# Kernel optimization log

Measured on AMD Instinct MI355X. Metric: run time of the kernel, lower is better.

## Reference

```python
import jax, jax.numpy as jnp
import numpy as np

B, S, E, H, L, OUT = 128, 256, 300, 512, 2, 2


def _lstm_dir(x, mask, w_ih, w_hh, b, h0, c0, reverse):
    """One direction of one LSTM layer with length masking (packed-seq semantics).
    x: [B,S,D], mask: [B,S] bool (t < length). Returns (outputs [B,S,H], final h [B,H]).
    For reverse=True, scan runs t=S-1..0; state only updates once t < length, which
    exactly reproduces pack_padded_sequence reverse-direction behavior.
    """
    def step(carry, inp):
        h, c = carry
        xt, mt = inp  # [B,D], [B]
        z = xt @ w_ih.T + h @ w_hh.T + b  # [B,4H], torch gate order i,f,g,o
        i, f, g, o = jnp.split(z, 4, axis=-1)
        c_new = jax.nn.sigmoid(f) * c + jax.nn.sigmoid(i) * jnp.tanh(g)
        h_new = jax.nn.sigmoid(o) * jnp.tanh(c_new)
        m = mt[:, None]
        h = jnp.where(m, h_new, h)
        c = jnp.where(m, c_new, c)
        return (h, c), h
    (hT, _), hs = jax.lax.scan(step, (h0, c0), (jnp.swapaxes(x, 0, 1), mask.T), reverse=reverse)
    return jnp.swapaxes(hs, 0, 1), hT


def setup_inputs():
    key = jax.random.key(0)
    ks = iter(jax.random.split(key, 32))
    lengths = jax.random.randint(next(ks), (B,), 1, S + 1)
    x = jax.random.normal(next(ks), (B, S, E), jnp.float32)
    # module encodes per-sample lengths in input[:, -1, 0]
    x = x.at[:, -1, 0].set(lengths.astype(jnp.float32))
    k = 1.0 / np.sqrt(H)
    def u(shape):
        return jax.random.uniform(next(ks), shape, jnp.float32, -k, k)
    d = {"x": x}
    for l in range(L):
        din = E if l == 0 else 2 * H
        for suf in ("f", "r"):
            d[f"w_ih_l{l}_{suf}"] = u((4 * H, din))
            d[f"w_hh_l{l}_{suf}"] = u((4 * H, H))
            d[f"b_ih_l{l}_{suf}"] = u((4 * H,))
            d[f"b_hh_l{l}_{suf}"] = u((4 * H,))
    d["fc1_w"] = u((H, H))
    d["fc1_b"] = u((H,))
    d["fc_w"] = u((OUT, H))
    d["fc_b"] = u((OUT,))
    return d


def _forward(x, params):
    Bx, Sx = x.shape[0], x.shape[1]
    lengths = jnp.minimum(x[:, -1, 0].astype(jnp.int32), Sx)  # clamp(max=seq_len)
    mask = jnp.arange(Sx)[None, :] < lengths[:, None]  # [B,S]
    h0 = jnp.ones((Bx, H), x.dtype)  # module uses ones, not zeros
    c0 = jnp.ones((Bx, H), x.dtype)
    inp = x
    hT_r = None
    for l in range(L):
        (wif, whf, bif, bhf), (wir, whr, bir, bhr) = params[l]
        out_f, _ = _lstm_dir(inp, mask, wif, whf, bif + bhf, h0, c0, False)
        out_r, hT_r = _lstm_dir(inp, mask, wir, whr, bir + bhr, h0, c0, True)
        inp = jnp.concatenate([out_f, out_r], axis=-1)  # [B,S,2H]
    # ht[-1] == final hidden of reverse direction of last layer
    return hT_r


def reference(x, w_ih_l0_f, w_hh_l0_f, b_ih_l0_f, b_hh_l0_f,
              w_ih_l0_r, w_hh_l0_r, b_ih_l0_r, b_hh_l0_r,
              w_ih_l1_f, w_hh_l1_f, b_ih_l1_f, b_hh_l1_f,
              w_ih_l1_r, w_hh_l1_r, b_ih_l1_r, b_hh_l1_r,
              fc1_w, fc1_b, fc_w, fc_b):
    params = [((w_ih_l0_f, w_hh_l0_f, b_ih_l0_f, b_hh_l0_f),
               (w_ih_l0_r, w_hh_l0_r, b_ih_l0_r, b_hh_l0_r)),
              ((w_ih_l1_f, w_hh_l1_f, b_ih_l1_f, b_hh_l1_f),
               (w_ih_l1_r, w_hh_l1_r, b_ih_l1_r, b_hh_l1_r))]
    ht = _forward(x, params)  # [B,H]
    out = ht @ fc1_w.T + fc1_b  # fc1 (no activation in original)
    return out @ fc_w.T + fc_b  # [B,OUT]
```

## Files before the change

kernel.cpp:

```cpp
#include <hip/hip_runtime.h>

#define B_  128
#define S_  256
#define E_  300
#define EP_ 320
#define H_  512
#define G_  2048
#define D1_ 1024
#define FSLOT_ 4
#define FA_WORDS_ (4*FSLOT_*4*32*32)
#define FC_WORDS_ (2*FSLOT_*4*32*32)

typedef _Float16 f16;
typedef __attribute__((ext_vector_type(8))) _Float16 f16x8;
typedef __attribute__((ext_vector_type(4))) float    f32x4;
typedef unsigned long long u64;
typedef unsigned int u32;

__device__ __forceinline__ float sigf(float x){ return 1.f/(1.f + __expf(-x)); }
__device__ __forceinline__ float tanhf_(float x){
  float e = __expf(-2.f*fabsf(x));
  float t = (1.f - e)/(1.f + e);
  return x < 0.f ? -t : t;
}

__device__ __forceinline__ u64 aload64(const u64* p){
  return __hip_atomic_load((u64*)p, __ATOMIC_RELAXED, __HIP_MEMORY_SCOPE_AGENT);
}
__device__ __forceinline__ u32 aload32(const u32* p){
  return __hip_atomic_load((u32*)p, __ATOMIC_RELAXED, __HIP_MEMORY_SCOPE_AGENT);
}
__device__ __forceinline__ void astore32(u32* p, u32 v){
  __hip_atomic_store(p, v, __ATOMIC_RELAXED, __HIP_MEMORY_SCOPE_AGENT);
}
union H8 { u64 q[2]; f16x8 v; };
union FU { f16 f; unsigned short s; };


__global__ void k_f32_to_f16(const float* __restrict__ s, f16* __restrict__ d, int n){
  int i = blockIdx.x*blockDim.x + threadIdx.x;
  if (i < n) d[i] = (f16)s[i];
}

__global__ void k_pad_w(const float* __restrict__ s, f16* __restrict__ d, int rows, int ks, int kd){
  int i = blockIdx.x*blockDim.x + threadIdx.x;
  if (i >= rows*kd) return;
  int r = i/kd, k = i - r*kd;
  d[i] = (k < ks) ? (f16)s[(size_t)r*ks + k] : (f16)0.f;
}

__global__ void k_bias(const float* __restrict__ a, const float* __restrict__ b,
                       float* __restrict__ d, int n){
  int i = blockIdx.x*blockDim.x + threadIdx.x;
  if (i < n) d[i] = a[i] + b[i];
}

__global__ void k_len(const float* __restrict__ x, int* __restrict__ len){
  int b = threadIdx.x;
  if (b < B_){
    int v = (int)x[((size_t)b*S_ + (S_-1))*E_];
    len[b] = v > S_ ? S_ : v;
  }
}

__global__ void k_zero(u32* __restrict__ p, int n){
  int i = blockIdx.x*blockDim.x + threadIdx.x;
  if (i < n) p[i] = 0u;
}

__global__ void k_init(f16* hxA, f16* hx1, float* cstate){
  int i = blockIdx.x*blockDim.x + threadIdx.x;
  if (i < B_*H_){
    hxA[i] = (f16)1.f;
    hxA[2*B_*H_ + i] = (f16)1.f;
    hx1[i] = (f16)1.f;
    cstate[i] = 1.f;
  }
}


__global__ __launch_bounds__(256) void k_gemm_bt(
    const f16* __restrict__ A, const f16* __restrict__ Bm,
    f16* __restrict__ C, const float* __restrict__ bias,
    int M, int N, int K)
{
  __shared__ f16 As[128*32];
  __shared__ f16 Bs[128*32];
  const int m0 = blockIdx.x*128, n0 = blockIdx.y*128;
  const int tid = threadIdx.x;
  const int w = tid>>6, lane = tid&63, quad = lane>>4, l16 = lane&15;
  const int wm = (w&1)*64, wn = (w>>1)*64;
  const int srow = w*32 + (lane>>2);
  const int scol = (lane&3)*8;
  const f16* Ap  = A  + (size_t)(m0 + srow)*K + scol;
  const f16* Bp  = Bm + (size_t)(n0 + srow)*K + scol;
  const f16* Ap2 = Ap + (size_t)16*K;
  const f16* Bp2 = Bp + (size_t)16*K;
  f16* ldsA  = &As[(w*32)*32];
  f16* ldsA2 = &As[(w*32+16)*32];
  f16* ldsB  = &Bs[(w*32)*32];
  f16* ldsB2 = &Bs[(w*32+16)*32];
  f32x4 z4 = {0.f,0.f,0.f,0.f};
  f32x4 acc[4][4];
#pragma unroll
  for (int mi = 0; mi < 4; ++mi)
#pragma unroll
    for (int ni = 0; ni < 4; ++ni) acc[mi][ni] = z4;

  for (int k0 = 0; k0 < K; k0 += 32){
    __builtin_amdgcn_global_load_lds(
        (const __attribute__((address_space(1))) void*)(Ap + k0),
        (__attribute__((address_space(3))) void*)ldsA, 16, 0, 0);
    __builtin_amdgcn_global_load_lds(
        (const __attribute__((address_space(1))) void*)(Ap2 + k0),
        (__attribute__((address_space(3))) void*)ldsA2, 16, 0, 0);
    __builtin_amdgcn_global_load_lds(
        (const __attribute__((address_space(1))) void*)(Bp + k0),
        (__attribute__((address_space(3))) void*)ldsB, 16, 0, 0);
    __builtin_amdgcn_global_load_lds(
        (const __attribute__((address_space(1))) void*)(Bp2 + k0),
        (__attribute__((address_space(3))) void*)ldsB2, 16, 0, 0);
    asm volatile("s_waitcnt vmcnt(0)" ::: "memory");
    __syncthreads();
    f16x8 a[4], b[4];
#pragma unroll
    for (int mi = 0; mi < 4; ++mi)
      a[mi] = *(const f16x8*)&As[(wm + mi*16 + l16)*32 + quad*8];
#pragma unroll
    for (int ni = 0; ni < 4; ++ni)
      b[ni] = *(const f16x8*)&Bs[(wn + ni*16 + l16)*32 + quad*8];
#pragma unroll
    for (int mi = 0; mi < 4; ++mi)
#pragma unroll
      for (int ni = 0; ni < 4; ++ni)
        acc[mi][ni] = __builtin_amdgcn_mfma_f32_16x16x32_f16(a[mi], b[ni], acc[mi][ni],0,0,0);
    __syncthreads();
  }
#pragma unroll
  for (int mi = 0; mi < 4; ++mi)
#pragma unroll
    for (int ni = 0; ni < 4; ++ni){
      int col = n0 + wn + ni*16 + l16;
      float bz = bias[col];
#pragma unroll
      for (int r = 0; r < 4; ++r){
        int row = m0 + wm + mi*16 + quad*4 + r;
        C[(size_t)row*N + col] = (f16)(acc[mi][ni][r] + bz);
      }
    }
}


__global__ __launch_bounds__(256, 1) void k_phaseA(
    const float* __restrict__ x,
    const f16* __restrict__ w0f, const f16* __restrict__ w0r,
    const f16* __restrict__ whf, const f16* __restrict__ whr,
    const float* __restrict__ bs0, const int* __restrict__ len,
    f16* __restrict__ hxA, f16* __restrict__ outcat,
    u32* __restrict__ flagsA)
{
  __shared__ f16 Wh[64*512];
  __shared__ f16 Wi[64*320];
  const int half = blockIdx.x, jb = blockIdx.y, dir = blockIdx.z;
  const f16* wih = dir ? w0r : w0f;
  const f16* whh = dir ? whr : whf;
  const float* bias = bs0 + dir*G_;
  f16* hx = hxA + (size_t)dir*(2*B_*H_);
  u32* fbase = flagsA + (size_t)(dir*2 + half)*(FSLOT_*4*32*32);
  const int tid = threadIdx.x;
  const int w = tid>>6, lane = tid&63, quad = lane>>4, l16 = lane&15;
  const int j0 = jb*16;
  const int m0 = half*64 + w*16;

  for (int u = tid; u < 4096; u += 256){
    int lrr = u>>6, uc = u&63;
    int g = lrr>>4, i = lrr&15;
    *(uint4*)&Wh[lrr*512 + (uc ^ (i&7))*8] =
        *(const uint4*)(whh + ((size_t)(g*H_ + j0 + i))*H_ + uc*8);
  }
  for (int u = tid; u < 2560; u += 256){
    int row = u/40, c = u - row*40;
    int g = row>>4, i = row&15;
    *(uint4*)&Wi[row*320 + (c ^ (i&7))*8] =
        *(const uint4*)(wih + ((size_t)(g*H_ + j0 + i))*EP_ + c*8);
  }
  __syncthreads();

  const int j = j0 + l16;
  float bz[4], hprev[4], cpr[4]; int lm[4];
#pragma unroll
  for (int g = 0; g < 4; ++g) bz[g] = bias[g*H_ + j];
#pragma unroll
  for (int r = 0; r < 4; ++r){ hprev[r] = 1.f; cpr[r] = 1.f; lm[r] = len[m0 + quad*4 + r]; }
  const size_t xrowbase = (size_t)(m0 + l16)*S_;

  float4 xA[9], xB[9]; float xT[8];
  {
    const int t0 = dir ? (S_-1) : 0;
    const float* xr = x + (xrowbase + t0)*E_;
#pragma unroll
    for (int kb = 0; kb < 9; ++kb){
      xA[kb] = *(const float4*)(xr + kb*32 + quad*8);
      xB[kb] = *(const float4*)(xr + kb*32 + quad*8 + 4);
    }
    int kbase = 288 + quad*8;
#pragma unroll
    for (int e2 = 0; e2 < 8; ++e2)
      xT[e2] = (kbase + e2 < E_) ? xr[kbase + e2] : 0.f;
  }

  for (int s = 0; s < S_; ++s){
    const int t = dir ? (S_-1-s) : s;
    f32x4 z4 = {0.f,0.f,0.f,0.f};
    f32x4 acc[4] = {z4,z4,z4,z4};

#pragma unroll
    for (int kb = 0; kb < 9; ++kb){
      f16x8 a;
      a[0]=(f16)xA[kb].x; a[1]=(f16)xA[kb].y; a[2]=(f16)xA[kb].z; a[3]=(f16)xA[kb].w;
      a[4]=(f16)xB[kb].x; a[5]=(f16)xB[kb].y; a[6]=(f16)xB[kb].z; a[7]=(f16)xB[kb].w;
      int c = (kb*4 + quad) ^ (l16 & 7);
#pragma unroll
      for (int g = 0; g < 4; ++g){
        f16x8 b = *(const f16x8*)&Wi[(g*16+l16)*320 + c*8];
        acc[g] = __builtin_amdgcn_mfma_f32_16x16x32_f16(a, b, acc[g],0,0,0);
      }
    }
    {
      f16x8 a;
#pragma unroll
      for (int e2 = 0; e2 < 8; ++e2) a[e2] = (f16)xT[e2];
      int c = (36 + quad) ^ (l16 & 7);
#pragma unroll
      for (int g = 0; g < 4; ++g){
        f16x8 b = *(const f16x8*)&Wi[(g*16+l16)*320 + c*8];
        acc[g] = __builtin_amdgcn_mfma_f32_16x16x32_f16(a, b, acc[g],0,0,0);
      }
    }

    if (s+1 < S_){
      const int tn = dir ? (S_-2-s) : (s+1);
      const float* xr = x + (xrowbase + tn)*E_;
#pragma unroll
      for (int kb = 0; kb < 9; ++kb){
        xA[kb] = *(const float4*)(xr + kb*32 + quad*8);
        xB[kb] = *(const float4*)(xr + kb*32 + quad*8 + 4);
      }
      int kbase = 288 + quad*8;
#pragma unroll
      for (int e2 = 0; e2 < 8; ++e2)
        xT[e2] = (kbase + e2 < E_) ? xr[kbase + e2] : 0.f;
    }

    if (s > 0){
      const u32* fp = fbase + ((size_t)((s-1)&(FSLOT_-1))*4 + w)*32*32;
      const u32 expv = (u32)s;
      for (;;){
        u32 v = aload32(fp + (size_t)(lane & 31)*32);
        if (__ballot(v == expv) == ~0ull) break;
      }
      asm volatile("" ::: "memory");
    }

    const int par = s & 1;
    const u64* hap = (const u64*)(hx + (size_t)par*(B_*H_) + (size_t)(m0 + l16)*H_);
    u64 hq[32];
#pragma unroll
    for (int kb = 0; kb < 16; ++kb){
      hq[2*kb]   = aload64(hap + kb*8 + quad*2);
      hq[2*kb+1] = aload64(hap + kb*8 + quad*2 + 1);
    }
#pragma unroll
    for (int kb = 0; kb < 16; ++kb){
      H8 ha;
      ha.q[0] = hq[2*kb];
      ha.q[1] = hq[2*kb+1];
      int uq = kb*4 + quad;
#pragma unroll
      for (int g = 0; g < 4; ++g){
        f16x8 b = *(const f16x8*)&Wh[(g*16+l16)*512 + ((uq ^ (l16&7)))*8];
        acc[g] = __builtin_amdgcn_mfma_f32_16x16x32_f16(ha.v, b, acc[g],0,0,0);
      }
    }

    f16* hn = hx + (size_t)(1-par)*(B_*H_);
#pragma unroll
    for (int r = 0; r < 4; ++r){
      int m = m0 + quad*4 + r;
      float zi = acc[0][r] + bz[0];
      float zf = acc[1][r] + bz[1];
      float zg = acc[2][r] + bz[2];
      float zo = acc[3][r] + bz[3];
      float ig = sigf(zi), fg = sigf(zf), gg = tanhf_(zg), og = sigf(zo);
      float cnew = fg*cpr[r] + ig*gg;
      float hnew = og*tanhf_(cnew);
      bool mk = t < lm[r];
      float hsel = mk ? hnew : hprev[r];
      cpr[r] = mk ? cnew : cpr[r];
      hprev[r] = hsel;
      FU cv; cv.f = (f16)hsel;
      int other = __shfl_down((int)cv.s, 1);
      if ((l16 & 1) == 0)
        astore32((u32*)(hn + (size_t)m*H_ + j), (u32)cv.s | ((u32)other << 16));
    }
    asm volatile("s_waitcnt vmcnt(0)" ::: "memory");
    if (lane == 0)
      astore32(fbase + (((size_t)(s&(FSLOT_-1))*4 + w)*32 + jb)*32, (u32)(s+1));

#pragma unroll
    for (int r = 0; r < 4; ++r){
      int m = m0 + quad*4 + r;
      FU cv; cv.f = (f16)hprev[r];
      int other = __shfl_down((int)cv.s, 1);
      if ((l16 & 1) == 0)
        *(u32*)(outcat + ((size_t)t*B_ + m)*D1_ + dir*H_ + j) = (u32)cv.s | ((u32)other << 16);
    }
  }
}


__global__ __launch_bounds__(256, 1) void k_phaseCrec(
    const f16* __restrict__ Z1c, const f16* __restrict__ w1h,
    const int* __restrict__ len,
    f16* __restrict__ hx1, float* __restrict__ cstate, float* __restrict__ h1f,
    u32* __restrict__ flagsC, int s0, int CH)
{
  __shared__ f16 Wh[64*512];
  const int half = blockIdx.x, jb = blockIdx.y;
  u32* fbase = flagsC + (size_t)half*(FSLOT_*4*32*32);
  const int tid = threadIdx.x;
  const int w = tid>>6, lane = tid&63, quad = lane>>4, l16 = lane&15;
  const int j0 = jb*16;
  const int m0 = half*64 + w*16;

  for (int u = tid; u < 4096; u += 256){
    int lrr = u>>6, uc = u&63;
    int g = lrr>>4, i = lrr&15;
    *(uint4*)&Wh[lrr*512 + (uc ^ (i&7))*8] =
        *(const uint4*)(w1h + ((size_t)(g*H_ + j0 + i))*H_ + uc*8);
  }
  __syncthreads();

  const int j = j0 + l16;
  float hprev[4], cpr[4]; int lm[4];
#pragma unroll
  for (int r = 0; r < 4; ++r){
    int m = m0 + quad*4 + r;
    lm[r] = len[m];
    cpr[r] = cstate[(size_t)m*H_ + j];
    hprev[r] = (float)hx1[(size_t)(s0 & 1)*(B_*H_) + (size_t)m*H_ + j];
  }

  for (int sl = 0; sl < CH; ++sl){
    const int s = s0 + sl;
    const int t = S_-1-s;
    const int zrow = CH-1-sl;

    float zv[4][4];
#pragma unroll
    for (int g = 0; g < 4; ++g)
#pragma unroll
      for (int r = 0; r < 4; ++r)
        zv[g][r] = (float)Z1c[((size_t)zrow*B_ + m0 + quad*4 + r)*G_ + g*H_ + j];

    if (s > 0){
      const u32* fp = fbase + ((size_t)((s-1)&(FSLOT_-1))*4 + w)*32*32;
      const u32 expv = (u32)s;
      for (;;){
        u32 v = aload32(fp + (size_t)(lane & 31)*32);
        if (__ballot(v == expv) == ~0ull) break;
      }
      asm volatile("" ::: "memory");
    }

    const int par = s & 1;
    const u64* hap = (const u64*)(hx1 + (size_t)par*(B_*H_) + (size_t)(m0 + l16)*H_);
    f32x4 z4 = {0.f,0.f,0.f,0.f};
    f32x4 acc[4] = {z4,z4,z4,z4};
    u64 hq[32];
#pragma unroll
    for (int kb = 0; kb < 16; ++kb){
      hq[2*kb]   = aload64(hap + kb*8 + quad*2);
      hq[2*kb+1] = aload64(hap + kb*8 + quad*2 + 1);
    }
#pragma unroll
    for (int kb = 0; kb < 16; ++kb){
      H8 ha;
      ha.q[0] = hq[2*kb];
      ha.q[1] = hq[2*kb+1];
      int uq = kb*4 + quad;
#pragma unroll
      for (int g = 0; g < 4; ++g){
        f16x8 b = *(const f16x8*)&Wh[(g*16+l16)*512 + ((uq ^ (l16&7)))*8];
        acc[g] = __builtin_amdgcn_mfma_f32_16x16x32_f16(ha.v, b, acc[g],0,0,0);
      }
    }

    f16* hn = hx1 + (size_t)(1-par)*(B_*H_);
#pragma unroll
    for (int r = 0; r < 4; ++r){
      int m = m0 + quad*4 + r;
      float zi = acc[0][r] + zv[0][r];
      float zf = acc[1][r] + zv[1][r];
      float zg = acc[2][r] + zv[2][r];
      float zo = acc[3][r] + zv[3][r];
      float ig = sigf(zi), fg = sigf(zf), gg = tanhf_(zg), og = sigf(zo);
      float cnew = fg*cpr[r] + ig*gg;
      float hnew = og*tanhf_(cnew);
      bool mk = t < lm[r];
      float hsel = mk ? hnew : hprev[r];
      cpr[r] = mk ? cnew : cpr[r];
      hprev[r] = hsel;
      FU cv; cv.f = (f16)hsel;
      int other = __shfl_down((int)cv.s, 1);
      if ((l16 & 1) == 0)
        astore32((u32*)(hn + (size_t)m*H_ + j), (u32)cv.s | ((u32)other << 16));
    }
    asm volatile("s_waitcnt vmcnt(0)" ::: "memory");
    if (lane == 0)
      astore32(fbase + (((size_t)(s&(FSLOT_-1))*4 + w)*32 + jb)*32, (u32)(s+1));

    if (t == 0){
#pragma unroll
      for (int r = 0; r < 4; ++r)
        h1f[(size_t)(m0 + quad*4 + r)*H_ + j] = hprev[r];
    }
  }

#pragma unroll
  for (int r = 0; r < 4; ++r)
    cstate[(size_t)(m0 + quad*4 + r)*H_ + j] = cpr[r];
}


__global__ void k_fold(const float* __restrict__ fc1w, const float* __restrict__ fc1b,
                       const float* __restrict__ fcw,  const float* __restrict__ fcb,
                       float* __restrict__ Mf, float* __restrict__ bf){
  int i = blockIdx.x*blockDim.x + threadIdx.x;
  if (i >= 1024) return;
  int o = i >> 9, h = i & 511;
  float s = 0.f;
  for (int jj = 0; jj < 512; ++jj) s += fcw[o*512 + jj] * fc1w[jj*512 + h];
  Mf[o*512 + h] = s;
  if (h == 0){
    float sb = fcb[o];
    for (int jj = 0; jj < 512; ++jj) sb += fcw[o*512 + jj] * fc1b[jj];
    bf[o] = sb;
  }
}

__global__ void k_final(const float* __restrict__ h1f, const float* __restrict__ Mf,
                        const float* __restrict__ bf, float* __restrict__ out){
  int i = threadIdx.x;
  if (i >= 256) return;
  int b = i >> 1, o = i & 1;
  float s = bf[o];
  const float* hp = h1f + (size_t)b*512;
  const float* mp = Mf + (size_t)o*512;
  for (int h = 0; h < 512; ++h) s += hp[h]*mp[h];
  out[b*2 + o] = s;
}


extern "C" void kernel_launch(void* const* d_in, const int* in_sizes, int n_in,
                              void* d_out, int out_size, void* d_ws, size_t ws_size,
                              hipStream_t stream)
{
  const float* x     = (const float*)d_in[0];
  const float* wih0f = (const float*)d_in[1];
  const float* whh0f = (const float*)d_in[2];
  const float* bih0f = (const float*)d_in[3];
  const float* bhh0f = (const float*)d_in[4];
  const float* wih0r = (const float*)d_in[5];
  const float* whh0r = (const float*)d_in[6];
  const float* bih0r = (const float*)d_in[7];
  const float* bhh0r = (const float*)d_in[8];
  const float* wih1r = (const float*)d_in[13];
  const float* whh1r = (const float*)d_in[14];
  const float* bih1r = (const float*)d_in[15];
  const float* bhh1r = (const float*)d_in[16];
  const float* fc1w  = (const float*)d_in[17];
  const float* fc1b  = (const float*)d_in[18];
  const float* fcw   = (const float*)d_in[19];
  const float* fcb   = (const float*)d_in[20];
  float* out = (float*)d_out;

  char* p = (char*)d_ws;
  auto alloc = [&](size_t bytes)->char*{
    char* r = p; p += (bytes + 255) & ~(size_t)255; return r;
  };
  f16* w0fp   = (f16*)alloc((size_t)G_*EP_*2);
  f16* w0rp   = (f16*)alloc((size_t)G_*EP_*2);
  f16* whf    = (f16*)alloc((size_t)G_*H_*2);
  f16* whr    = (f16*)alloc((size_t)G_*H_*2);
  f16* w1i    = (f16*)alloc((size_t)G_*D1_*2);
  f16* w1h    = (f16*)alloc((size_t)G_*H_*2);
  float* bs0  = (float*)alloc((size_t)2*G_*4);
  float* bs1r = (float*)alloc(G_*4);
  int*   len  = (int*)alloc(B_*4);
  f16* outcat = (f16*)alloc((size_t)S_*B_*D1_*2);
  f16* hxA    = (f16*)alloc((size_t)2*2*B_*H_*2);
  f16* hx1    = (f16*)alloc((size_t)2*B_*H_*2);
  float* cstate=(float*)alloc((size_t)B_*H_*4);
  float* h1f  = (float*)alloc((size_t)B_*H_*4);
  float* Mf   = (float*)alloc(2*512*4);
  float* bf   = (float*)alloc(256);
  u32* flagsA = (u32*)alloc((size_t)FA_WORDS_*4);
  u32* flagsC = (u32*)alloc((size_t)FC_WORDS_*4);
  size_t used = (size_t)(p - (char*)d_ws);
  int CH = 8;
  for (int c = 256; c >= 8; c >>= 1){
    if (used + (size_t)c*B_*G_*2 <= ws_size){ CH = c; break; }
  }
  f16* Z1c = (f16*)alloc((size_t)CH*B_*G_*2);
  const int NC = S_/CH;

  int n;
  n = G_*EP_; k_pad_w<<<(n+255)/256, 256, 0, stream>>>(wih0f, w0fp, G_, E_, EP_);
              k_pad_w<<<(n+255)/256, 256, 0, stream>>>(wih0r, w0rp, G_, E_, EP_);
  n = G_*H_;  k_f32_to_f16<<<(n+255)/256,256,0,stream>>>(whh0f, whf, n);
              k_f32_to_f16<<<(n+255)/256,256,0,stream>>>(whh0r, whr, n);
              k_f32_to_f16<<<(n+255)/256,256,0,stream>>>(whh1r, w1h, n);
  n = G_*D1_; k_f32_to_f16<<<(n+255)/256,256,0,stream>>>(wih1r, w1i, n);
  k_bias<<<8,256,0,stream>>>(bih0f, bhh0f, bs0, G_);
  k_bias<<<8,256,0,stream>>>(bih0r, bhh0r, bs0 + G_, G_);
  k_bias<<<8,256,0,stream>>>(bih1r, bhh1r, bs1r, G_);
  k_len<<<1,128,0,stream>>>(x, len);
  k_init<<<(B_*H_+255)/256,256,0,stream>>>(hxA, hx1, cstate);
  k_zero<<<(FA_WORDS_+255)/256,256,0,stream>>>(flagsA, FA_WORDS_);
  k_zero<<<(FC_WORDS_+255)/256,256,0,stream>>>(flagsC, FC_WORDS_);
  k_fold<<<4,256,0,stream>>>(fc1w, fc1b, fcw, fcb, Mf, bf);

  k_phaseA<<<dim3(2,32,2), 256, 0, stream>>>(
      x, w0fp, w0rp, whf, whr, bs0, len, hxA, outcat, flagsA);

  for (int cc = 0; cc < NC; ++cc){
    int t0 = S_ - (cc+1)*CH;
    k_gemm_bt<<<dim3(CH, 16), 256, 0, stream>>>(
        outcat + (size_t)t0*B_*D1_, w1i, Z1c, bs1r, CH*B_, G_, D1_);
    k_phaseCrec<<<dim3(2,32), 256, 0, stream>>>(
        Z1c, w1h, len, hx1, cstate, h1f, flagsC, cc*CH, CH);
  }

  k_final<<<1,256,0,stream>>>(h1f, Mf, bf, out);
}
```

Baseline: 3.978 ms.

## Hoist layer-0 input projection into one batched GEMM before the recurrence

Casts x to padded fp16 and computes the layer-0 input-gate projections for all timesteps and both directions with a single large GEMM, with the biases folded in. The recurrent kernel then only does the h@W_hh MFMA each step and reads the precomputed gate pre-activations, so the input matmul leaves the sequential critical path. The same large buffer is reused as the layer-1 projection buffer, so layer 1 runs as one chunk. The cost is a large fp16 intermediate written and read through strided per-step loads. The GEMM also assumes the forward and reverse padded weights sit next to each other in the workspace.

```diff
diff --git a/kernel.cpp b/kernel.cpp
--- a/kernel.cpp
+++ b/kernel.cpp
@@ -7,6 +7,7 @@
 #define H_  512
 #define G_  2048
 #define D1_ 1024
+#define G2_ 4096
 #define FSLOT_ 4
 #define FA_WORDS_ (4*FSLOT_*4*32*32)
 #define FC_WORDS_ (2*FSLOT_*4*32*32)
@@ -47,6 +48,14 @@
   if (i >= rows*kd) return;
   int r = i/kd, k = i - r*kd;
   d[i] = (k < ks) ? (f16)s[(size_t)r*ks + k] : (f16)0.f;
+}
+
+__global__ void k_cast_x(const float* __restrict__ x, f16* __restrict__ xf){
+  int i = blockIdx.x*blockDim.x + threadIdx.x;
+  if (i >= S_*B_*EP_) return;
+  int e = i % EP_; int rm = i / EP_;
+  int m = rm % B_; int t = rm / B_;
+  xf[i] = (e < E_) ? (f16)x[((size_t)m*S_ + t)*E_ + e] : (f16)0.f;
 }
 
 __global__ void k_bias(const float* __restrict__ a, const float* __restrict__ b,
@@ -152,7 +161,7 @@
 
 
 __global__ __launch_bounds__(256, 1) void k_phaseA(
-    const float* __restrict__ x,
+    const float* __restrict__ x, const f16* __restrict__ xz,
     const f16* __restrict__ w0f, const f16* __restrict__ w0r,
     const f16* __restrict__ whf, const f16* __restrict__ whr,
     const float* __restrict__ bs0, const int* __restrict__ len,
@@ -178,11 +187,13 @@
     *(uint4*)&Wh[lrr*512 + (uc ^ (i&7))*8] =
         *(const uint4*)(whh + ((size_t)(g*H_ + j0 + i))*H_ + uc*8);
   }
-  for (int u = tid; u < 2560; u += 256){
-    int row = u/40, c = u - row*40;
-    int g = row>>4, i = row&15;
-    *(uint4*)&Wi[row*320 + (c ^ (i&7))*8] =
-        *(const uint4*)(wih + ((size_t)(g*H_ + j0 + i))*EP_ + c*8);
+  if (!xz){
+    for (int u = tid; u < 2560; u += 256){
+      int row = u/40, c = u - row*40;
+      int g = row>>4, i = row&15;
+      *(uint4*)&Wi[row*320 + (c ^ (i&7))*8] =
+          *(const uint4*)(wih + ((size_t)(g*H_ + j0 + i))*EP_ + c*8);
+    }
   }
   __syncthreads();
 
@@ -193,6 +204,87 @@
 #pragma unroll
   for (int r = 0; r < 4; ++r){ hprev[r] = 1.f; cpr[r] = 1.f; lm[r] = len[m0 + quad*4 + r]; }
   const size_t xrowbase = (size_t)(m0 + l16)*S_;
+
+  if (xz){
+    for (int s = 0; s < S_; ++s){
+      const int t = dir ? (S_-1-s) : s;
+
+      const f16* zr = xz + ((size_t)t*B_)*G2_ + dir*G_;
+      float zvv[4][4];
+#pragma unroll
+      for (int g = 0; g < 4; ++g)
+#pragma unroll
+        for (int r = 0; r < 4; ++r)
+          zvv[g][r] = (float)zr[(size_t)(m0 + quad*4 + r)*G2_ + g*H_ + j];
+
+      if (s > 0){
+        const u32* fp = fbase + ((size_t)((s-1)&(FSLOT_-1))*4 + w)*32*32;
+        const u32 expv = (u32)s;
+        for (;;){
+          u32 v = aload32(fp + (size_t)(lane & 31)*32);
+          if (__ballot(v == expv) == ~0ull) break;
+        }
+        asm volatile("" ::: "memory");
+      }
+
+      const int par = s & 1;
+      const u64* hap = (const u64*)(hx + (size_t)par*(B_*H_) + (size_t)(m0 + l16)*H_);
+      f32x4 z4 = {0.f,0.f,0.f,0.f};
+      f32x4 acc[4] = {z4,z4,z4,z4};
+      u64 hq[32];
+#pragma unroll
+      for (int kb = 0; kb < 16; ++kb){
+        hq[2*kb]   = aload64(hap + kb*8 + quad*2);
+        hq[2*kb+1] = aload64(hap + kb*8 + quad*2 + 1);
+      }
+#pragma unroll
+      for (int kb = 0; kb < 16; ++kb){
+        H8 ha;
+        ha.q[0] = hq[2*kb];
+        ha.q[1] = hq[2*kb+1];
+        int uq = kb*4 + quad;
+#pragma unroll
+        for (int g = 0; g < 4; ++g){
+          f16x8 b = *(const f16x8*)&Wh[(g*16+l16)*512 + ((uq ^ (l16&7)))*8];
+          acc[g] = __builtin_amdgcn_mfma_f32_16x16x32_f16(ha.v, b, acc[g],0,0,0);
+        }
+      }
+
+      f16* hn = hx + (size_t)(1-par)*(B_*H_);
+#pragma unroll
+      for (int r = 0; r < 4; ++r){
+        int m = m0 + quad*4 + r;
+        float zi = acc[0][r] + zvv[0][r];
+        float zf = acc[1][r] + zvv[1][r];
+        float zg = acc[2][r] + zvv[2][r];
+        float zo = acc[3][r] + zvv[3][r];
+        float ig = sigf(zi), fg = sigf(zf), gg = tanhf_(zg), og = sigf(zo);
+        float cnew = fg*cpr[r] + ig*gg;
+        float hnew = og*tanhf_(cnew);
+        bool mk = t < lm[r];
+        float hsel = mk ? hnew : hprev[r];
+        cpr[r] = mk ? cnew : cpr[r];
+        hprev[r] = hsel;
+        FU cv; cv.f = (f16)hsel;
+        int other = __shfl_down((int)cv.s, 1);
+        if ((l16 & 1) == 0)
+          astore32((u32*)(hn + (size_t)m*H_ + j), (u32)cv.s | ((u32)other << 16));
+      }
+      asm volatile("s_waitcnt vmcnt(0)" ::: "memory");
+      if (lane == 0)
+        astore32(fbase + (((size_t)(s&(FSLOT_-1))*4 + w)*32 + jb)*32, (u32)(s+1));
+
+#pragma unroll
+      for (int r = 0; r < 4; ++r){
+        int m = m0 + quad*4 + r;
+        FU cv; cv.f = (f16)hprev[r];
+        int other = __shfl_down((int)cv.s, 1);
+        if ((l16 & 1) == 0)
+          *(u32*)(outcat + ((size_t)t*B_ + m)*D1_ + dir*H_ + j) = (u32)cv.s | ((u32)other << 16);
+      }
+    }
+    return;
+  }
 
   float4 xA[9], xB[9]; float xT[8];
   {
@@ -508,11 +600,22 @@
   u32* flagsA = (u32*)alloc((size_t)FA_WORDS_*4);
   u32* flagsC = (u32*)alloc((size_t)FC_WORDS_*4);
   size_t used = (size_t)(p - (char*)d_ws);
-  int CH = 8;
-  for (int c = 256; c >= 8; c >>= 1){
-    if (used + (size_t)c*B_*G_*2 <= ws_size){ CH = c; break; }
-  }
-  f16* Z1c = (f16*)alloc((size_t)CH*B_*G_*2);
+
+  const size_t XZ_BYTES = (size_t)S_*B_*G2_*2;
+  const size_t XF_BYTES = (size_t)S_*B_*EP_*2;
+  f16* Xz = nullptr; f16* xf = nullptr; f16* Z1c; int CH;
+  if (used + XZ_BYTES + XF_BYTES + 512 <= ws_size){
+    Xz  = (f16*)alloc(XZ_BYTES);
+    xf  = (f16*)alloc(XF_BYTES);
+    Z1c = Xz;
+    CH  = 256;
+  } else {
+    CH = 8;
+    for (int c = 256; c >= 8; c >>= 1){
+      if (used + (size_t)c*B_*G_*2 <= ws_size){ CH = c; break; }
+    }
+    Z1c = (f16*)alloc((size_t)CH*B_*G_*2);
+  }
   const int NC = S_/CH;
 
   int n;
@@ -531,8 +634,15 @@
   k_zero<<<(FC_WORDS_+255)/256,256,0,stream>>>(flagsC, FC_WORDS_);
   k_fold<<<4,256,0,stream>>>(fc1w, fc1b, fcw, fcb, Mf, bf);
 
+  if (Xz){
+    n = S_*B_*EP_;
+    k_cast_x<<<(n+255)/256, 256, 0, stream>>>(x, xf);
+    k_gemm_bt<<<dim3(S_*B_/128, G2_/128), 256, 0, stream>>>(
+        xf, w0fp, Xz, bs0, S_*B_, G2_, EP_);
+  }
+
   k_phaseA<<<dim3(2,32,2), 256, 0, stream>>>(
-      x, w0fp, w0rp, whf, whr, bs0, len, hxA, outcat, flagsA);
+      x, Xz, w0fp, w0rp, whf, whr, bs0, len, hxA, outcat, flagsA);
 
   for (int cc = 0; cc < NC; ++cc){
     int t0 = S_ - (cc+1)*CH;
```

New measurement: 3.971 ms. About the same (-0.2%).
